# Kernel tuning notes

Hardware: AMD Instinct MI355X
Metric: run time of the kernel (lower is better)

The kernel has to match this reference:

```python
import jax, jax.numpy as jnp
import numpy as np

B, S, D, V = 2, 2048, 1024, 50257
GAMMA = 1.0
IGNORE = -100


def setup_inputs() -> dict:
    key = jax.random.key(0)
    k1, k2, k3, k4 = jax.random.split(key, 4)
    embeddings = jax.random.normal(k1, (B, S, D), dtype=jnp.float32)
    W = jax.random.normal(k2, (V, D), dtype=jnp.float32) * (D ** -0.5)
    b = jnp.zeros((V,), dtype=jnp.float32)
    labels = jax.random.randint(k3, (B, S), 0, V, dtype=jnp.int64)
    input_ids = jax.random.randint(k4, (B, S), 0, V, dtype=jnp.int64)
    return {"embeddings": embeddings, "W": W, "b": b, "labels": labels, "input_ids": input_ids}


def _focal_loss(embeddings, W, b, labels):
    # logits: [B, S, V]
    logits = jnp.einsum('bsd,vd->bsv', embeddings, W) + b
    shift_logits = logits[:, :-1, :].reshape(-1, V)          # [N, V]
    shift_labels = labels[:, 1:].reshape(-1)                  # [N]
    valid = shift_labels != IGNORE
    safe = jnp.where(valid, shift_labels, 0)
    logp = jax.nn.log_softmax(shift_logits, axis=-1)
    ce = -jnp.take_along_axis(logp, safe[:, None], axis=-1)[:, 0]
    ce = jnp.where(valid, ce, 0.0)                            # ignore_index -> 0 loss
    pt = jax.lax.stop_gradient(jnp.exp(-ce))
    w = (1.0 - pt) ** GAMMA
    alpha = 1.0 / jnp.mean(w)
    loss = alpha * w * ce
    return jnp.mean(loss)


def reference(embeddings, W, b, labels, input_ids):
    return _focal_loss(embeddings, W, b, labels)
```

## Files before the change

### kernel.cpp

```cpp
#include <hip/hip_runtime.h>
#include <hip/hip_bf16.h>
#include <cstdint>

#define SDIM   2048
#define DDIM   1024
#define VDIM   50257
#define VPAD   50432
#define NROWS  4094
#define MPAD   4096
#define NTM    16
#define NTN    197
#define NCHUNK (NTN * 4)
#define NKT    16
#define IGNORE_IDX (-100)
#define NEGBIG (-3.0e38f)
#define SLICE_SH 8192

typedef __bf16 bf16x8 __attribute__((ext_vector_type(8)));
typedef float  f32x4  __attribute__((ext_vector_type(4)));

__device__ static inline unsigned short f2bf(float f) {
    union { float f; uint32_t u; } v; v.f = f;
    uint32_t u = v.u;
    return (unsigned short)((u + 0x7FFFu + ((u >> 16) & 1u)) >> 16);
}

__device__ static inline void gload_lds16(const void* g, void* l) {
    __builtin_amdgcn_global_load_lds(
        (const __attribute__((address_space(1))) unsigned int*)(g),
        (__attribute__((address_space(3))) unsigned int*)(l),
        16, 0, 0);
}

__global__ __launch_bounds__(256) void k_convert_W(const float* __restrict__ W,
                                                   unsigned short* __restrict__ Wb,
                                                   float* __restrict__ acc) {
    if (blockIdx.x == 0 && threadIdx.x < 2) acc[threadIdx.x] = 0.f;
    const int nf4 = VPAD * (DDIM / 4);
    for (int i = blockIdx.x * 256 + threadIdx.x; i < nf4; i += gridDim.x * 256) {
        const int row = i >> 8;
        const int c4  = (i & 255) << 2;
        ushort4 o;
        if (row < VDIM) {
            const float4 f = *(const float4*)(W + (size_t)row * DDIM + c4);
            o.x = f2bf(f.x); o.y = f2bf(f.y); o.z = f2bf(f.z); o.w = f2bf(f.w);
        } else {
            o.x = o.y = o.z = o.w = 0;
        }
        *(ushort4*)(Wb + (size_t)row * DDIM + c4) = o;
    }
}

__global__ __launch_bounds__(256) void k_convert_A(const float* __restrict__ emb,
                                                   unsigned short* __restrict__ Ab) {
    const int nf4 = MPAD * (DDIM / 4);
    for (int i = blockIdx.x * 256 + threadIdx.x; i < nf4; i += gridDim.x * 256) {
        const int row = i >> 8;
        const int c4  = (i & 255) << 2;
        ushort4 o; o.x = o.y = o.z = o.w = 0;
        if (row < NROWS) {
            const int bb = row / 2047;
            const int s  = row - bb * 2047;
            const float4 f = *(const float4*)(emb + ((size_t)bb * SDIM + s) * DDIM + c4);
            o.x = f2bf(f.x); o.y = f2bf(f.y); o.z = f2bf(f.z); o.w = f2bf(f.w);
        }
        *(ushort4*)(Ab + (size_t)row * DDIM + c4) = o;
    }
}

__global__ __launch_bounds__(512, 2) void k_gemm(const unsigned short* __restrict__ Ab,
                                                 const unsigned short* __restrict__ Wb,
                                                 const float* __restrict__ bias,
                                                 float2* __restrict__ Pml) {
    extern __shared__ unsigned short lds[];
    unsigned short* As = lds;
    unsigned short* Bs = lds + 4 * SLICE_SH;

    const int tid  = threadIdx.x;
    const int wave = tid >> 6, lane = tid & 63;
    const int q    = lane & 15, g = lane >> 4;
    const int wr   = wave >> 2;
    const int wc   = wave & 3;

    const int bid0 = (int)blockIdx.x;
    const int bid  = (bid0 & 7) * (NTM * NTN / 8) + (bid0 >> 3);
    const int tm   = bid & 15;
    const int tn   = bid >> 4;
    const size_t arow0 = (size_t)tm * 256;
    const size_t brow0 = (size_t)tn * 256;

    f32x4 acc[8][4];
    const f32x4 zf = {0.f, 0.f, 0.f, 0.f};
#pragma unroll
    for (int i = 0; i < 8; ++i)
#pragma unroll
        for (int j = 0; j < 4; ++j) acc[i][j] = zf;

    auto stage_slice = [&](int bufIdx, int kt, int s) {
        unsigned short* LA = As + (bufIdx * 2 + s) * SLICE_SH;
        unsigned short* LB = Bs + (bufIdx * 2 + s) * SLICE_SH;
#pragma unroll
        for (int j = 0; j < 2; ++j) {
            const int ci  = j * 512 + tid;
            const int row = ((ci >> 3) << 1) + ((ci >> 2) & 1);
            const int cs  = (ci & 3) ^ ((ci >> 3) & 3);
            const size_t goff = (size_t)kt * 64 + s * 32 + cs * 8;
            unsigned short* ldst = (unsigned short*)((size_t)(j * 512 + wave * 64) * 8);
            gload_lds16(Ab + (arow0 + row) * DDIM + goff, LA + (size_t)(j * 512 + wave * 64) * 8);
            gload_lds16(Wb + (brow0 + row) * DDIM + goff, LB + (size_t)(j * 512 + wave * 64) * 8);
            (void)ldst;
        }
    };

    auto lds_frag = [&](const unsigned short* SL, int row) -> bf16x8 {
        const int line = row >> 1;
        const int p    = ((row & 1) << 2) + (g ^ (line & 3));
        return *(const bf16x8*)(SL + line * 64 + p * 8);
    };

    auto do_phase = [&](int c, int mh, int ks, int stageT, int vm, bool tileEndBar) {
        if (stageT >= 0) stage_slice(c ^ 1, stageT, ks);
        if (vm == 8)      { asm volatile("s_waitcnt vmcnt(8)" ::: "memory"); }
        else if (vm == 4) { asm volatile("s_waitcnt vmcnt(4)" ::: "memory"); }
        else if (vm == 0) { asm volatile("s_waitcnt vmcnt(0)" ::: "memory"); }
        if (vm >= 0) {
            __builtin_amdgcn_sched_barrier(0);
            __builtin_amdgcn_s_barrier();
        }
        const unsigned short* SA = As + (c * 2 + ks) * SLICE_SH;
        const unsigned short* SB = Bs + (c * 2 + ks) * SLICE_SH;
        bf16x8 af[4], bfr[4];
#pragma unroll
        for (int fi = 0; fi < 4; ++fi)
            af[fi] = lds_frag(SA, wr * 128 + mh * 64 + fi * 16 + q);
#pragma unroll
        for (int fj = 0; fj < 4; ++fj)
            bfr[fj] = lds_frag(SB, wc * 64 + fj * 16 + q);
        asm volatile("s_waitcnt lgkmcnt(0)" ::: "memory");
        __builtin_amdgcn_sched_barrier(0);
        if (tileEndBar) __builtin_amdgcn_s_barrier();
        __builtin_amdgcn_s_setprio(1);
#pragma unroll
        for (int fi = 0; fi < 4; ++fi)
#pragma unroll
            for (int fj = 0; fj < 4; ++fj)
                acc[mh * 4 + fi][fj] = __builtin_amdgcn_mfma_f32_16x16x32_bf16(
                    af[fi], bfr[fj], acc[mh * 4 + fi][fj], 0, 0, 0);
        __builtin_amdgcn_s_setprio(0);
        __builtin_amdgcn_sched_barrier(0);
    };

    stage_slice(0, 0, 0);
    stage_slice(0, 0, 1);

#pragma unroll 1
    for (int t = 0; t < NKT - 1; ++t) {
        const int c = t & 1;
        do_phase(c, 0, 0, t + 1, 8, false);
        do_phase(c, 1, 0, -1, -1, false);
        do_phase(c, 0, 1, t + 1, 8, false);
        do_phase(c, 1, 1, -1, -1, true);
    }
    {
        const int c = (NKT - 1) & 1;
        do_phase(c, 0, 0, -1, 4, false);
        do_phase(c, 1, 0, -1, -1, false);
        do_phase(c, 0, 1, -1, 0, false);
        do_phase(c, 1, 1, -1, -1, false);
    }

    float bv[4]; int colv[4];
#pragma unroll
    for (int fj = 0; fj < 4; ++fj) {
        const int col = tn * 256 + wc * 64 + fj * 16 + q;
        colv[fj] = col;
        bv[fj] = (col < VDIM) ? bias[col] : 0.f;
    }
#pragma unroll
    for (int mf = 0; mf < 8; ++mf) {
#pragma unroll
        for (int r = 0; r < 4; ++r) {
            float vv[4];
#pragma unroll
            for (int fj = 0; fj < 4; ++fj) {
                const float lv = acc[mf][fj][r] + bv[fj];
                vv[fj] = (colv[fj] < VDIM) ? lv : NEGBIG;
            }
            float m = fmaxf(fmaxf(vv[0], vv[1]), fmaxf(vv[2], vv[3]));
#pragma unroll
            for (int mask = 1; mask < 16; mask <<= 1) m = fmaxf(m, __shfl_xor(m, mask));
            float s = __expf(vv[0] - m) + __expf(vv[1] - m) +
                      __expf(vv[2] - m) + __expf(vv[3] - m);
#pragma unroll
            for (int mask = 1; mask < 16; mask <<= 1) s += __shfl_xor(s, mask);
            if (q == ((mf * 4 + r) & 15)) {
                const int rowg = tm * 256 + wr * 128 + mf * 16 + g * 4 + r;
                Pml[(size_t)rowg * NCHUNK + (tn * 4 + wc)] = make_float2(m, s);
            }
        }
    }
}

__global__ __launch_bounds__(256) void k_finalize(const float2* __restrict__ Pml,
                                                  const float* __restrict__ emb,
                                                  const float* __restrict__ W,
                                                  const float* __restrict__ bias,
                                                  const int* __restrict__ labels,
                                                  float* __restrict__ acc) {
    const int r    = blockIdx.x;
    const int tid  = threadIdx.x;
    const int lane = tid & 63, wave = tid >> 6;

    float m = NEGBIG, l = 0.f;
    for (int c = tid; c < NCHUNK; c += 256) {
        const float2 p = Pml[(size_t)r * NCHUNK + c];
        const float mn = fmaxf(m, p.x);
        l = l * __expf(m - mn) + p.y * __expf(p.x - mn);
        m = mn;
    }
#pragma unroll
    for (int mask = 1; mask < 64; mask <<= 1) {
        const float om = __shfl_xor(m, mask);
        const float ol = __shfl_xor(l, mask);
        const float mn = fmaxf(m, om);
        l = l * __expf(m - mn) + ol * __expf(om - mn);
        m = mn;
    }

    const int bb = r / 2047;
    const int s  = r - bb * 2047;
    const int label = labels[bb * SDIM + s + 1];
    const bool valid = (label != IGNORE_IDX);
    const int lab = valid ? label : 0;
    const float* erow = emb + ((size_t)bb * SDIM + s) * DDIM;
    const float* wrow = W + (size_t)lab * DDIM;
    const float4 e  = *(const float4*)(erow + tid * 4);
    const float4 w4 = *(const float4*)(wrow + tid * 4);
    float d = e.x * w4.x + e.y * w4.y + e.z * w4.z + e.w * w4.w;
#pragma unroll
    for (int mask = 1; mask < 64; mask <<= 1) d += __shfl_xor(d, mask);

    __shared__ float sm[4], sl[4], sd[4];
    if (lane == 0) { sm[wave] = m; sl[wave] = l; sd[wave] = d; }
    __syncthreads();
    if (tid == 0) {
        float M = sm[0], L = sl[0];
#pragma unroll
        for (int wv = 1; wv < 4; ++wv) {
            const float mn = fmaxf(M, sm[wv]);
            L = L * __expf(M - mn) + sl[wv] * __expf(sm[wv] - mn);
            M = mn;
        }
        const float dot = sd[0] + sd[1] + sd[2] + sd[3];
        const float lse = M + logf(L);
        const float logit = dot + bias[lab];
        const float ce = valid ? (lse - logit) : 0.f;
        const float pt = __expf(-ce);
        const float w  = valid ? (1.f - pt) : 0.f;
        atomicAdd(acc + 0, w * ce);
        atomicAdd(acc + 1, w);
    }
}

__global__ void k_final(const float* __restrict__ acc, float* __restrict__ out) {
    out[0] = acc[0] / acc[1];
}

extern "C" void kernel_launch(void* const* d_in, const int* in_sizes, int n_in,
                              void* d_out, int out_size, void* d_ws, size_t ws_size,
                              hipStream_t stream) {
    const float* emb    = (const float*)d_in[0];
    const float* W      = (const float*)d_in[1];
    const float* bias   = (const float*)d_in[2];
    const int*   labels = (const int*)d_in[3];

    char* ws = (char*)d_ws;
    const size_t WB = (size_t)VPAD * DDIM * 2;
    const size_t AB = (size_t)MPAD * DDIM * 2;
    const size_t PB = (size_t)MPAD * NCHUNK * 8;
    unsigned short* Wb  = (unsigned short*)ws;
    unsigned short* Ab  = (unsigned short*)(ws + WB);
    float2*         Pml = (float2*)(ws + WB + AB);
    float*          acc = (float*)(ws + WB + AB + PB);

    k_convert_W<<<2048, 256, 0, stream>>>(W, Wb, acc);
    k_convert_A<<<1024, 256, 0, stream>>>(emb, Ab);
    k_gemm<<<NTM * NTN, 512, 131072, stream>>>(Ab, Wb, bias, Pml);
    k_finalize<<<NROWS, 256, 0, stream>>>(Pml, emb, W, bias, labels, acc);
    k_final<<<1, 1, 0, stream>>>(acc, (float*)d_out);
}
```

Baseline: 944.1 us.

## Restructure GEMM K-loop into deeper slice-level prefetch pipeline with reordered barriers

The GEMM main loop is rewritten so that global-to-LDS loads for upcoming K slices are issued after the LDS fragment reads of each phase, with three slices in flight instead of a whole next tile. vmcnt waits and barriers move to the end of each phase, and the loop is unrolled over two buffers. This aims to hide global-load latency behind MFMA work at a finer granularity, at the cost of a barrier every phase and tighter buffer-reuse hazards. The conversion kernels also switch from grid-stride loops to one block per row.

```diff
diff --git a/kernel.cpp b/kernel.cpp
--- a/kernel.cpp
+++ b/kernel.cpp
@@ -36,36 +36,30 @@
                                                    unsigned short* __restrict__ Wb,
                                                    float* __restrict__ acc) {
     if (blockIdx.x == 0 && threadIdx.x < 2) acc[threadIdx.x] = 0.f;
-    const int nf4 = VPAD * (DDIM / 4);
-    for (int i = blockIdx.x * 256 + threadIdx.x; i < nf4; i += gridDim.x * 256) {
-        const int row = i >> 8;
-        const int c4  = (i & 255) << 2;
-        ushort4 o;
-        if (row < VDIM) {
-            const float4 f = *(const float4*)(W + (size_t)row * DDIM + c4);
-            o.x = f2bf(f.x); o.y = f2bf(f.y); o.z = f2bf(f.z); o.w = f2bf(f.w);
-        } else {
-            o.x = o.y = o.z = o.w = 0;
-        }
-        *(ushort4*)(Wb + (size_t)row * DDIM + c4) = o;
-    }
+    const int row = blockIdx.x;
+    const int c4  = threadIdx.x << 2;
+    ushort4 o;
+    if (row < VDIM) {
+        const float4 f = *(const float4*)(W + (size_t)row * DDIM + c4);
+        o.x = f2bf(f.x); o.y = f2bf(f.y); o.z = f2bf(f.z); o.w = f2bf(f.w);
+    } else {
+        o.x = o.y = o.z = o.w = 0;
+    }
+    *(ushort4*)(Wb + (size_t)row * DDIM + c4) = o;
 }
 
 __global__ __launch_bounds__(256) void k_convert_A(const float* __restrict__ emb,
                                                    unsigned short* __restrict__ Ab) {
-    const int nf4 = MPAD * (DDIM / 4);
-    for (int i = blockIdx.x * 256 + threadIdx.x; i < nf4; i += gridDim.x * 256) {
-        const int row = i >> 8;
-        const int c4  = (i & 255) << 2;
-        ushort4 o; o.x = o.y = o.z = o.w = 0;
-        if (row < NROWS) {
-            const int bb = row / 2047;
-            const int s  = row - bb * 2047;
-            const float4 f = *(const float4*)(emb + ((size_t)bb * SDIM + s) * DDIM + c4);
-            o.x = f2bf(f.x); o.y = f2bf(f.y); o.z = f2bf(f.z); o.w = f2bf(f.w);
-        }
-        *(ushort4*)(Ab + (size_t)row * DDIM + c4) = o;
-    }
+    const int row = blockIdx.x;
+    const int c4  = threadIdx.x << 2;
+    ushort4 o; o.x = o.y = o.z = o.w = 0;
+    if (row < NROWS) {
+        const int bb = row / 2047;
+        const int s  = row - bb * 2047;
+        const float4 f = *(const float4*)(emb + ((size_t)bb * SDIM + s) * DDIM + c4);
+        o.x = f2bf(f.x); o.y = f2bf(f.y); o.z = f2bf(f.z); o.w = f2bf(f.w);
+    }
+    *(ushort4*)(Ab + (size_t)row * DDIM + c4) = o;
 }
 
 __global__ __launch_bounds__(512, 2) void k_gemm(const unsigned short* __restrict__ Ab,
@@ -96,7 +90,8 @@
 #pragma unroll
         for (int j = 0; j < 4; ++j) acc[i][j] = zf;
 
-    auto stage_slice = [&](int bufIdx, int kt, int s) {
+    auto stage_slice = [&](int kt, int s) {
+        const int bufIdx = kt & 1;
         unsigned short* LA = As + (bufIdx * 2 + s) * SLICE_SH;
         unsigned short* LB = Bs + (bufIdx * 2 + s) * SLICE_SH;
 #pragma unroll
@@ -105,10 +100,9 @@
             const int row = ((ci >> 3) << 1) + ((ci >> 2) & 1);
             const int cs  = (ci & 3) ^ ((ci >> 3) & 3);
             const size_t goff = (size_t)kt * 64 + s * 32 + cs * 8;
-            unsigned short* ldst = (unsigned short*)((size_t)(j * 512 + wave * 64) * 8);
-            gload_lds16(Ab + (arow0 + row) * DDIM + goff, LA + (size_t)(j * 512 + wave * 64) * 8);
-            gload_lds16(Wb + (brow0 + row) * DDIM + goff, LB + (size_t)(j * 512 + wave * 64) * 8);
-            (void)ldst;
+            const size_t ldst = (size_t)(j * 512 + wave * 64) * 8;
+            gload_lds16(Ab + (arow0 + row) * DDIM + goff, LA + ldst);
+            gload_lds16(Wb + (brow0 + row) * DDIM + goff, LB + ldst);
         }
     };
 
@@ -118,17 +112,9 @@
         return *(const bf16x8*)(SL + line * 64 + p * 8);
     };
 
-    auto do_phase = [&](int c, int mh, int ks, int stageT, int vm, bool tileEndBar) {
-        if (stageT >= 0) stage_slice(c ^ 1, stageT, ks);
-        if (vm == 8)      { asm volatile("s_waitcnt vmcnt(8)" ::: "memory"); }
-        else if (vm == 4) { asm volatile("s_waitcnt vmcnt(4)" ::: "memory"); }
-        else if (vm == 0) { asm volatile("s_waitcnt vmcnt(0)" ::: "memory"); }
-        if (vm >= 0) {
-            __builtin_amdgcn_sched_barrier(0);
-            __builtin_amdgcn_s_barrier();
-        }
-        const unsigned short* SA = As + (c * 2 + ks) * SLICE_SH;
-        const unsigned short* SB = Bs + (c * 2 + ks) * SLICE_SH;
+    auto phase = [&](int bt, int mh, int ks, int stKt, int stS, int vm) {
+        const unsigned short* SA = As + (bt * 2 + ks) * SLICE_SH;
+        const unsigned short* SB = Bs + (bt * 2 + ks) * SLICE_SH;
         bf16x8 af[4], bfr[4];
 #pragma unroll
         for (int fi = 0; fi < 4; ++fi)
@@ -136,9 +122,11 @@
 #pragma unroll
         for (int fj = 0; fj < 4; ++fj)
             bfr[fj] = lds_frag(SB, wc * 64 + fj * 16 + q);
+        if (stKt >= 0) stage_slice(stKt, stS);
+        __builtin_amdgcn_sched_barrier(0);
+        __builtin_amdgcn_s_barrier();
         asm volatile("s_waitcnt lgkmcnt(0)" ::: "memory");
         __builtin_amdgcn_sched_barrier(0);
-        if (tileEndBar) __builtin_amdgcn_s_barrier();
         __builtin_amdgcn_s_setprio(1);
 #pragma unroll
         for (int fi = 0; fi < 4; ++fi)
@@ -148,25 +136,40 @@
                     af[fi], bfr[fj], acc[mh * 4 + fi][fj], 0, 0, 0);
         __builtin_amdgcn_s_setprio(0);
         __builtin_amdgcn_sched_barrier(0);
+        if (vm == 8)      { asm volatile("s_waitcnt vmcnt(8)" ::: "memory"); __builtin_amdgcn_sched_barrier(0); }
+        else if (vm == 4) { asm volatile("s_waitcnt vmcnt(4)" ::: "memory"); __builtin_amdgcn_sched_barrier(0); }
+        else if (vm == 0) { asm volatile("s_waitcnt vmcnt(0)" ::: "memory"); __builtin_amdgcn_sched_barrier(0); }
+        __builtin_amdgcn_s_barrier();
     };
 
-    stage_slice(0, 0, 0);
-    stage_slice(0, 0, 1);
+    stage_slice(0, 0);
+    stage_slice(0, 1);
+    stage_slice(1, 0);
+    asm volatile("s_waitcnt vmcnt(8)" ::: "memory");
+    __builtin_amdgcn_sched_barrier(0);
+    __builtin_amdgcn_s_barrier();
 
 #pragma unroll 1
-    for (int t = 0; t < NKT - 1; ++t) {
-        const int c = t & 1;
-        do_phase(c, 0, 0, t + 1, 8, false);
-        do_phase(c, 1, 0, -1, -1, false);
-        do_phase(c, 0, 1, t + 1, 8, false);
-        do_phase(c, 1, 1, -1, -1, true);
+    for (int i = 0; i < 7; ++i) {
+        const int t = 2 * i;
+        phase(0, 0, 0, t + 1, 1, -1);
+        phase(0, 1, 0, -1, 0, 8);
+        phase(0, 0, 1, t + 2, 0, -1);
+        phase(0, 1, 1, -1, 0, 8);
+        phase(1, 0, 0, t + 2, 1, -1);
+        phase(1, 1, 0, -1, 0, 8);
+        phase(1, 0, 1, t + 3, 0, -1);
+        phase(1, 1, 1, -1, 0, 8);
     }
     {
-        const int c = (NKT - 1) & 1;
-        do_phase(c, 0, 0, -1, 4, false);
-        do_phase(c, 1, 0, -1, -1, false);
-        do_phase(c, 0, 1, -1, 0, false);
-        do_phase(c, 1, 1, -1, -1, false);
+        phase(0, 0, 0, 15, 1, -1);
+        phase(0, 1, 0, -1, 0, 8);
+        phase(0, 0, 1, -1, 0, -1);
+        phase(0, 1, 1, -1, 0, 4);
+        phase(1, 0, 0, -1, 0, -1);
+        phase(1, 1, 0, -1, 0, 0);
+        phase(1, 0, 1, -1, 0, -1);
+        phase(1, 1, 1, -1, 0, -1);
     }
 
     float bv[4]; int colv[4];
@@ -283,8 +286,8 @@
     float2*         Pml = (float2*)(ws + WB + AB);
     float*          acc = (float*)(ws + WB + AB + PB);
 
-    k_convert_W<<<2048, 256, 0, stream>>>(W, Wb, acc);
-    k_convert_A<<<1024, 256, 0, stream>>>(emb, Ab);
+    k_convert_W<<<VPAD, 256, 0, stream>>>(W, Wb, acc);
+    k_convert_A<<<MPAD, 256, 0, stream>>>(emb, Ab);
     k_gemm<<<NTM * NTN, 512, 131072, stream>>>(Ab, Wb, bias, Pml);
     k_finalize<<<NROWS, 256, 0, stream>>>(Pml, emb, W, bias, labels, acc);
     k_final<<<1, 1, 0, stream>>>(acc, (float*)d_out);
```

Result: no change. 954.5 us (+1.1%).
